# Kernel tuning notes

Measured on AMD Instinct MI355X. Metric: run time of the kernel, lower is better.

Reference implementation:

```python
import jax, jax.numpy as jnp
import numpy as np

HIDDEN = 256

def setup_inputs() -> dict:
    key = jax.random.key(0)
    ks = jax.random.split(key, 8)
    B, N1, N2, D = 4, 4096, 4096, 256
    s = 1.0 / np.sqrt(D)
    return {
        "inputs1": jax.random.normal(ks[0], (B, N1, D), jnp.float32),
        "inputs2": jax.random.normal(ks[1], (B, N2, D), jnp.float32),
        "mask": jax.random.randint(ks[2], (B, N1, N2), 0, 2, jnp.int32),
        "Wq": jax.random.normal(ks[3], (D, HIDDEN), jnp.float32) * s,
        "bq": jnp.zeros((HIDDEN,), jnp.float32),
        "Wk": jax.random.normal(ks[4], (D, HIDDEN), jnp.float32) * s,
        "bk": jnp.zeros((HIDDEN,), jnp.float32),
        "Wv": jax.random.normal(ks[5], (D, HIDDEN), jnp.float32) * s,
        "bv": jnp.zeros((HIDDEN,), jnp.float32),
    }

def reference(inputs1, inputs2, mask, Wq, bq, Wk, bk, Wv, bv):
    # q: (B,N1,H), k,v: (B,N2,H)
    q = inputs1 @ Wq + bq
    k = inputs2 @ Wk + bk
    v = inputs2 @ Wv + bv
    scale = 1.0 / np.sqrt(HIDDEN)
    # scores: (B,N1,N2)
    scores = jnp.einsum('bnh,bmh->bnm', q, k) * scale
    # original: masked_fill(mask <= 0, 1e-9) -- NOT -inf; replicate faithfully
    scores = jnp.where(mask <= 0, jnp.float32(1e-9), scores)
    attn = jax.nn.softmax(scores, axis=-1)
    return jnp.einsum('bnm,bmh->bnh', attn, v)
```

## Files before the change

kernel.cpp:

```cpp
#include <hip/hip_runtime.h>

typedef float  f32x4 __attribute__((ext_vector_type(4)));
typedef short  s16x8 __attribute__((ext_vector_type(8)));
typedef short  s16x4 __attribute__((ext_vector_type(4)));

#define MFMA16(a,b,c) __builtin_amdgcn_mfma_f32_16x16x32_bf16(a,b,c,0,0,0)

static __device__ __forceinline__ f32x4 mfma_pv(s16x4 a, s16x4 b, f32x4 c){
#if defined(__HIP_DEVICE_COMPILE__)
    return __builtin_amdgcn_mfma_f32_16x16x16bf16_1k(a, b, c, 0, 0, 0);
#else
    (void)a; (void)b; return c;
#endif
}

static __device__ __forceinline__ void glds16(const void* g, void* l){
#if defined(__HIP_DEVICE_COMPILE__)
    __builtin_amdgcn_global_load_lds(
        (const __attribute__((address_space(1))) unsigned int*)g,
        (__attribute__((address_space(3))) unsigned int*)l, 16, 0, 0);
#else
    (void)g; (void)l;
#endif
}

static __device__ __forceinline__ unsigned short f2bf(float f){
    union { float f; unsigned int u; } x; x.f = f;
    unsigned int r = x.u + 0x7fffu + ((x.u >> 16) & 1u);
    return (unsigned short)(r >> 16);
}

__global__ void wt_prep(const float* __restrict__ Wq, const float* __restrict__ Wk,
                        const float* __restrict__ Wv, unsigned short* __restrict__ wt){
    const int p = blockIdx.y;
    const int o8 = blockIdx.x*256 + threadIdx.x;
    const float* W = (p==0) ? Wq : ((p==1) ? Wk : Wv);
    const int lane = o8 & 63, t = (o8 >> 6) & 15, ks = o8 >> 10;
    const int quad = lane >> 4, lq = lane & 15;
    s16x8 o;
    #pragma unroll
    for(int j=0;j<8;j++)
        o[j] = (short)f2bf(W[(ks*32 + quad*8 + j)*256 + 16*t + lq]);
    *(s16x8*)(wt + (size_t)p*65536 + (size_t)o8*8) = o;
}

static __device__ __forceinline__ void stage_x(const float* x, size_t row0,
                                               int tid, unsigned short* sX){
    const float* xg = x + row0*256;
    #pragma unroll
    for(int rr=0; rr<16; rr++){
        int c = tid + rr*256;
        int row = c>>6, cc = c&63;
        float4 f = *(const float4*)(xg + row*256 + cc*4);
        unsigned short* d = &sX[row*264 + cc*4];
        d[0]=f2bf(f.x); d[1]=f2bf(f.y); d[2]=f2bf(f.z); d[3]=f2bf(f.w);
    }
}

__global__ __launch_bounds__(256) void proj_all(const float* __restrict__ x1,
        const float* __restrict__ x2, const unsigned short* __restrict__ wt,
        const float* __restrict__ bq, const float* __restrict__ bk,
        const float* __restrict__ bv, int b0,
        unsigned short* __restrict__ qdst, unsigned short* __restrict__ kfrag,
        unsigned short* __restrict__ vfrag){
    const int rt = blockIdx.x, p = blockIdx.y, z = blockIdx.z;
    const int zz = b0 + z;
    const int tid = threadIdx.x, w = tid>>6, lane = tid&63, quad = lane>>4, lq = lane&15;
    __shared__ __align__(16) unsigned short sX[64*264];

    const float* x = (p==0) ? x1 : x2;
    stage_x(x, (size_t)(zz*64 + rt)*64, tid, sX);
    __syncthreads();

    s16x8 a[8];
    #pragma unroll
    for(int ks=0; ks<8; ks++)
        a[ks] = *(const s16x8*)(&sX[(16*w+lq)*264 + ks*32 + quad*8]);

    f32x4 acc[16];
    #pragma unroll
    for(int t=0;t<16;t++) acc[t] = (f32x4)(0.0f);
    const unsigned short* wtp = wt + (size_t)p*65536;
    #pragma unroll
    for(int ks=0; ks<8; ks++){
        #pragma unroll
        for(int t=0; t<16; t++){
            s16x8 bf_ = *(const s16x8*)(wtp + (((size_t)(ks*16 + t)*64 + lane)*8));
            acc[t] = MFMA16(a[ks], bf_, acc[t]);
        }
    }

    if(p == 0){
        #pragma unroll
        for(int t=0;t<16;t++){
            float bvf = bq[16*t+lq];
            #pragma unroll
            for(int r=0;r<4;r++){
                size_t row = (size_t)(zz*64 + rt)*64 + 16*w + 4*quad + r;
                qdst[row*256 + 16*t + lq] = f2bf(acc[t][r] + bvf);
            }
        }
    } else if(p == 1){
        __syncthreads();
        #pragma unroll
        for(int t=0;t<16;t++){
            float bvf = bk[16*t+lq];
            #pragma unroll
            for(int r=0;r<4;r++)
                sX[(16*w + 4*quad + r)*264 + 16*t + lq] = f2bf(acc[t][r] + bvf);
        }
        __syncthreads();
        unsigned short* kd = kfrag + (size_t)z*1048576;
        #pragma unroll
        for(int ks=0; ks<8; ks++){
            s16x8 v = *(const s16x8*)(&sX[(16*w + lq)*264 + 32*ks + 8*quad]);
            *(s16x8*)(kd + ((((size_t)rt*4 + w)*8 + ks)*64 + lane)*8) = v;
        }
    } else {
        unsigned short* vd = vfrag + (size_t)z*1048576;
        #pragma unroll
        for(int t2=0; t2<8; t2++){
            float b0f = bv[16*(2*t2  )+lq];
            float b1f = bv[16*(2*t2+1)+lq];
            s16x8 o;
            #pragma unroll
            for(int r=0;r<4;r++){
                o[r]   = (short)f2bf(acc[2*t2  ][r] + b0f);
                o[4+r] = (short)f2bf(acc[2*t2+1][r] + b1f);
            }
            *(s16x8*)(vd + ((((size_t)rt*4 + w)*8 + t2)*64 + lane)*8) = o;
        }
    }
}

__global__ __launch_bounds__(512,2) void attn(
        const unsigned short* __restrict__ qb, const unsigned short* __restrict__ kfrag,
        const unsigned short* __restrict__ vfrag, const int* __restrict__ mask,
        float* __restrict__ out, int b0){
    const int bid = blockIdx.x;
    int b, qt, bk_;
    if(gridDim.x == 256){ b = (bid&7)>>1; qt = (bid>>3)*2 + (bid&1); bk_ = b; }
    else                { b = b0; qt = bid; bk_ = 0; }
    const int tid = threadIdx.x, w4 = tid>>6, lane = tid&63, quad = lane>>4, lq = lane&15;
    const int qg = w4>>2, w = w4&3;
    const int qbase = qt*64 + 32*qg;

    __shared__ __align__(16) unsigned char smem[131072];

    s16x8 qf[2][8];
    #pragma unroll
    for(int rg=0; rg<2; rg++){
        size_t row = (size_t)(b*4096 + qbase + 16*rg + lq);
        #pragma unroll
        for(int ks=0; ks<8; ks++)
            qf[rg][ks] = *(const s16x8*)(qb + row*256 + ks*32 + quad*8);
    }

    f32x4 oacc[16][2];
    #pragma unroll
    for(int t=0;t<16;t++){ oacc[t][0] = (f32x4)(0.0f); oacc[t][1] = (f32x4)(0.0f); }
    float rsum[2] = {0.0f, 0.0f};

    const unsigned char* kfb = (const unsigned char*)(kfrag + (size_t)bk_*1048576);
    const unsigned char* vfb = (const unsigned char*)(vfrag + (size_t)bk_*1048576);
    const int* mp0 = mask + ((size_t)(b*4096 + qbase) + lq)*4096 + 16*w + 4*quad;
    const unsigned lsl = w4*1024 + lane*16;
    const unsigned ldd = w4*1024;

    int4 mA0 = *(const int4*)(mp0);
    int4 mA1 = *(const int4*)(mp0 + (size_t)16*4096);
    #pragma unroll
    for(int r=0; r<4; r++){
        glds16(kfb + r*8192 + lsl, smem + r*8192 + ldd);
        glds16(vfb + r*8192 + lsl, smem + 32768 + r*8192 + ldd);
    }
    int4 mN0 = mA0, mN1 = mA1;

    for(int kt=0; kt<64; kt++){
        const int cb = kt & 1;
        __syncthreads();
        if(kt < 63){
            mN0 = *(const int4*)(mp0 + (size_t)(kt+1)*64);
            mN1 = *(const int4*)(mp0 + (size_t)16*4096 + (kt+1)*64);
            const unsigned char* gK = kfb + (size_t)(kt+1)*32768;
            const unsigned char* gV = vfb + (size_t)(kt+1)*32768;
            unsigned char* dst = smem + (cb^1)*65536;
            #pragma unroll
            for(int r=0; r<4; r++){
                glds16(gK + r*8192 + lsl, dst + r*8192 + ldd);
                glds16(gV + r*8192 + lsl, dst + 32768 + r*8192 + ldd);
            }
        }
        const unsigned short* bK = (const unsigned short*)(smem + cb*65536);
        const unsigned short* bV = (const unsigned short*)(smem + cb*65536 + 32768);

        f32x4 sacc0 = (f32x4)(0.0f), sacc1 = (f32x4)(0.0f);
        #pragma unroll
        for(int ks=0; ks<8; ks++){
            s16x8 kf = *(const s16x8*)(bK + ((w*8 + ks)*64 + lane)*8);
            sacc0 = MFMA16(kf, qf[0][ks], sacc0);
            sacc1 = MFMA16(kf, qf[1][ks], sacc1);
        }
        s16x4 pb0, pb1;
        {
            float p;
            p = (mA0.x>0)?__expf(sacc0[0]*0.0625f):1.0f; rsum[0]+=p; pb0[0]=(short)f2bf(p);
            p = (mA0.y>0)?__expf(sacc0[1]*0.0625f):1.0f; rsum[0]+=p; pb0[1]=(short)f2bf(p);
            p = (mA0.z>0)?__expf(sacc0[2]*0.0625f):1.0f; rsum[0]+=p; pb0[2]=(short)f2bf(p);
            p = (mA0.w>0)?__expf(sacc0[3]*0.0625f):1.0f; rsum[0]+=p; pb0[3]=(short)f2bf(p);
            p = (mA1.x>0)?__expf(sacc1[0]*0.0625f):1.0f; rsum[1]+=p; pb1[0]=(short)f2bf(p);
            p = (mA1.y>0)?__expf(sacc1[1]*0.0625f):1.0f; rsum[1]+=p; pb1[1]=(short)f2bf(p);
            p = (mA1.z>0)?__expf(sacc1[2]*0.0625f):1.0f; rsum[1]+=p; pb1[2]=(short)f2bf(p);
            p = (mA1.w>0)?__expf(sacc1[3]*0.0625f):1.0f; rsum[1]+=p; pb1[3]=(short)f2bf(p);
        }
        #pragma unroll
        for(int t2=0; t2<8; t2++){
            s16x8 vv = *(const s16x8*)(bV + ((w*8 + t2)*64 + lane)*8);
            s16x4 vlo = __builtin_shufflevector(vv, vv, 0,1,2,3);
            s16x4 vhi = __builtin_shufflevector(vv, vv, 4,5,6,7);
            oacc[2*t2  ][0] = mfma_pv(vlo, pb0, oacc[2*t2  ][0]);
            oacc[2*t2  ][1] = mfma_pv(vlo, pb1, oacc[2*t2  ][1]);
            oacc[2*t2+1][0] = mfma_pv(vhi, pb0, oacc[2*t2+1][0]);
            oacc[2*t2+1][1] = mfma_pv(vhi, pb1, oacc[2*t2+1][1]);
        }
        mA0 = mN0; mA1 = mN1;
    }

    float* sRS  = (float*)smem;
    float* sRed = (float*)(smem + 1024);
    #pragma unroll
    for(int rg=0; rg<2; rg++){
        float v = rsum[rg];
        v += __shfl_xor(v, 16);
        v += __shfl_xor(v, 32);
        if(quad == 0) sRS[(qg*4 + w)*32 + 16*rg + lq] = v;
    }
    for(int g=0; g<2; g++){
        for(int c=0; c<4; c++){
            __syncthreads();
            if(qg == g){
                #pragma unroll
                for(int tt=0; tt<4; tt++){
                    int t = 4*c + tt;
                    #pragma unroll
                    for(int rg=0; rg<2; rg++){
                        #pragma unroll
                        for(int r=0; r<4; r++)
                            sRed[w*2081 + (16*rg+lq)*65 + 16*tt + 4*quad + r] = oacc[t][rg][r];
                    }
                }
            }
            __syncthreads();
            #pragma unroll
            for(int j=0; j<4; j++){
                int idx = j*512 + tid;
                int hl = idx & 63, q = idx >> 6;
                float s  = sRed[0*2081 + q*65+hl] + sRed[1*2081 + q*65+hl]
                         + sRed[2*2081 + q*65+hl] + sRed[3*2081 + q*65+hl];
                float rs = sRS[(g*4+0)*32+q] + sRS[(g*4+1)*32+q]
                         + sRS[(g*4+2)*32+q] + sRS[(g*4+3)*32+q];
                out[((size_t)(b*4096 + qt*64 + 32*g + q))*256 + 64*c + hl] = s / rs;
            }
        }
    }
}

extern "C" void kernel_launch(void* const* d_in, const int* in_sizes, int n_in,
                              void* d_out, int out_size, void* d_ws, size_t ws_size,
                              hipStream_t stream){
    (void)in_sizes; (void)n_in; (void)out_size;
    const float* x1 = (const float*)d_in[0];
    const float* x2 = (const float*)d_in[1];
    const int*   mk = (const int*)  d_in[2];
    const float* Wq = (const float*)d_in[3];
    const float* bq = (const float*)d_in[4];
    const float* Wk = (const float*)d_in[5];
    const float* bk = (const float*)d_in[6];
    const float* Wv = (const float*)d_in[7];
    const float* bv = (const float*)d_in[8];
    float* out = (float*)d_out;
    char* ws = (char*)d_ws;

    unsigned short* wt = (unsigned short*)ws;
    unsigned short* qb = (unsigned short*)(ws + 393216);
    const size_t kvoff = 393216 + 8388608;

    wt_prep<<<dim3(32,3), 256, 0, stream>>>(Wq, Wk, Wv, wt);

    if(ws_size >= kvoff + 16ull*1024*1024){
        unsigned short* kf = (unsigned short*)(ws + kvoff);
        unsigned short* vf = (unsigned short*)(ws + kvoff + 8388608);
        proj_all<<<dim3(64,3,4), 256, 0, stream>>>(x1, x2, wt, bq, bk, bv, 0,
                                                   qb, kf, vf);
        attn<<<256, 512, 0, stream>>>(qb, kf, vf, mk, out, 0);
    } else {
        unsigned short* kf = (unsigned short*)(ws + kvoff);
        unsigned short* vf = (unsigned short*)(ws + kvoff + 2097152);
        for(int b=0;b<4;b++){
            proj_all<<<dim3(64,3,1), 256, 0, stream>>>(x1, x2, wt, bq, bk, bv, b,
                                                       qb, kf, vf);
            attn<<<64, 512, 0, stream>>>(qb, kf, vf, mk, out, b);
        }
    }
}
```

Baseline: 499.4 us.

## Stream V directly to registers and triple-buffer K tiles in LDS

Removes V from the LDS staging path, so each wave loads its V fragments straight from global memory into registers every iteration. K tiles are now triple-buffered in LDS with a two-tile prefetch distance, synchronised by an explicit vmcnt wait and s_barrier. This cuts LDS use and the ds_read traffic for V, and aims to overlap loads more deeply. In exchange it uses more VGPRs and duplicates V global reads across the two query groups, and the hand-tuned vmcnt count is fragile.

```diff
diff --git a/kernel.cpp b/kernel.cpp
--- a/kernel.cpp
+++ b/kernel.cpp
@@ -145,7 +145,7 @@
     const int qg = w4>>2, w = w4&3;
     const int qbase = qt*64 + 32*qg;
 
-    __shared__ __align__(16) unsigned char smem[131072];
+    __shared__ __align__(16) unsigned char smem[98304];
 
     s16x8 qf[2][8];
     #pragma unroll
@@ -167,33 +167,49 @@
     const unsigned lsl = w4*1024 + lane*16;
     const unsigned ldd = w4*1024;
 
+    #pragma unroll
+    for(int r=0; r<4; r++)
+        glds16(kfb + r*8192 + lsl, smem + r*8192 + ldd);
+    __builtin_amdgcn_sched_barrier(0);
     int4 mA0 = *(const int4*)(mp0);
     int4 mA1 = *(const int4*)(mp0 + (size_t)16*4096);
-    #pragma unroll
-    for(int r=0; r<4; r++){
-        glds16(kfb + r*8192 + lsl, smem + r*8192 + ldd);
-        glds16(vfb + r*8192 + lsl, smem + 32768 + r*8192 + ldd);
-    }
-    int4 mN0 = mA0, mN1 = mA1;
+    __builtin_amdgcn_sched_barrier(0);
+    #pragma unroll
+    for(int r=0; r<4; r++)
+        glds16(kfb + 32768 + r*8192 + lsl, smem + 32768 + r*8192 + ldd);
 
     for(int kt=0; kt<64; kt++){
-        const int cb = kt & 1;
-        __syncthreads();
+        const unsigned bufb = (unsigned)(kt % 3) * 32768u;
+        __builtin_amdgcn_sched_barrier(0);
+        asm volatile("s_waitcnt vmcnt(6)" ::: "memory");
+        __builtin_amdgcn_s_barrier();
+        __builtin_amdgcn_sched_barrier(0);
+
+        s16x8 vf_[8];
+        {
+            const unsigned char* gV = vfb + (size_t)kt*32768;
+            #pragma unroll
+            for(int t2=0; t2<8; t2++)
+                vf_[t2] = *(const s16x8*)(gV + (((unsigned)(w*8 + t2)*64 + lane)*16));
+        }
+        int4 mN0 = mA0, mN1 = mA1;
         if(kt < 63){
             mN0 = *(const int4*)(mp0 + (size_t)(kt+1)*64);
             mN1 = *(const int4*)(mp0 + (size_t)16*4096 + (kt+1)*64);
-            const unsigned char* gK = kfb + (size_t)(kt+1)*32768;
-            const unsigned char* gV = vfb + (size_t)(kt+1)*32768;
-            unsigned char* dst = smem + (cb^1)*65536;
-            #pragma unroll
-            for(int r=0; r<4; r++){
-                glds16(gK + r*8192 + lsl, dst + r*8192 + ldd);
-                glds16(gV + r*8192 + lsl, dst + 32768 + r*8192 + ldd);
-            }
-        }
-        const unsigned short* bK = (const unsigned short*)(smem + cb*65536);
-        const unsigned short* bV = (const unsigned short*)(smem + cb*65536 + 32768);
-
+        }
+        __builtin_amdgcn_sched_barrier(0);
+
+        if(kt < 63){
+            const int st = (kt < 62) ? (kt+2) : 63;
+            const unsigned sb = (unsigned)((kt+2) % 3) * 32768u;
+            const unsigned char* gK = kfb + (size_t)st*32768;
+            #pragma unroll
+            for(int r=0; r<4; r++)
+                glds16(gK + r*8192 + lsl, smem + sb + r*8192 + ldd);
+        }
+        __builtin_amdgcn_sched_barrier(0);
+
+        const unsigned short* bK = (const unsigned short*)(smem + bufb);
         f32x4 sacc0 = (f32x4)(0.0f), sacc1 = (f32x4)(0.0f);
         #pragma unroll
         for(int ks=0; ks<8; ks++){
@@ -215,9 +231,8 @@
         }
         #pragma unroll
         for(int t2=0; t2<8; t2++){
-            s16x8 vv = *(const s16x8*)(bV + ((w*8 + t2)*64 + lane)*8);
-            s16x4 vlo = __builtin_shufflevector(vv, vv, 0,1,2,3);
-            s16x4 vhi = __builtin_shufflevector(vv, vv, 4,5,6,7);
+            s16x4 vlo = __builtin_shufflevector(vf_[t2], vf_[t2], 0,1,2,3);
+            s16x4 vhi = __builtin_shufflevector(vf_[t2], vf_[t2], 4,5,6,7);
             oacc[2*t2  ][0] = mfma_pv(vlo, pb0, oacc[2*t2  ][0]);
             oacc[2*t2  ][1] = mfma_pv(vlo, pb1, oacc[2*t2  ][1]);
             oacc[2*t2+1][0] = mfma_pv(vhi, pb0, oacc[2*t2+1][0]);
@@ -226,6 +241,7 @@
         mA0 = mN0; mA1 = mN1;
     }
 
+    __syncthreads();
     float* sRS  = (float*)smem;
     float* sRed = (float*)(smem + 1024);
     #pragma unroll
```

Result: slower. 629.9 us (+26.1%).
